# Performance work log

Measured on AMD Instinct MI355X. Metric: run time of the kernel, lower is better.

The kernel has to match this reference:

```python
import jax, jax.numpy as jnp
import numpy as np

K = 15
LAM = 1.0
EPS = 1e-8


def _pdist(a):
    # pairwise euclidean distance (torch.cdist p=2), safe sqrt (zero grad at 0)
    sq = jnp.sum(a * a, axis=1)
    d2 = sq[:, None] + sq[None, :] - 2.0 * (a @ a.T)
    d2 = jnp.maximum(d2, 0.0)
    pos = d2 > 0
    return jnp.where(pos, jnp.sqrt(jnp.where(pos, d2, 1.0)), 0.0)


def _knn_distance_loss(z, xf, k):
    B = xf.shape[0]
    x_dist = _pdist(xf)
    z_dist = _pdist(z)
    eye = jnp.eye(B, dtype=bool)
    x_noself = jnp.where(eye, jnp.inf, x_dist)
    # k smallest per row -> top_k of negated distances
    _, knn_idx = jax.lax.top_k(-x_noself, k)          # (B, k)
    rows = jnp.arange(B)[:, None]
    mask = jnp.zeros((B, B), dtype=bool).at[rows, knn_idx].set(True)
    mask = mask | mask.T                              # symmetric kNN mask
    x_m = jnp.where(mask, x_dist, 0.0)
    z_m = jnp.where(mask, z_dist, 0.0)
    x_norm = x_m / (jnp.max(x_m) + EPS)
    z_norm = z_m / (jnp.max(z_m) + EPS)
    diff2 = jnp.where(mask, (z_norm - x_norm) ** 2, 0.0)
    return diff2.sum() / mask.sum().astype(diff2.dtype)


def _forward(x, We1, be1, We2, be2, Wd1, bd1, Wd2, bd2):
    h = jax.nn.relu(x @ We1 + be1)
    z = h @ We2 + be2                                  # (B, latent)
    h2 = jax.nn.relu(z @ Wd1 + bd1)
    x_rec = h2 @ Wd2 + bd2
    rec_loss = jnp.mean((x_rec - x) ** 2)
    dist_loss = _knn_distance_loss(z, x.reshape(x.shape[0], -1), K)
    return rec_loss + LAM * dist_loss


def setup_inputs() -> dict:
    key = jax.random.key(0)
    ks = jax.random.split(key, 5)
    B, D, H, L = 8192, 1024, 512, 64
    s = 0.02
    return {
        "x": jax.random.normal(ks[0], (B, D), dtype=jnp.float32),
        "We1": jax.random.normal(ks[1], (D, H), dtype=jnp.float32) * s,
        "be1": jnp.zeros((H,), dtype=jnp.float32),
        "We2": jax.random.normal(ks[2], (H, L), dtype=jnp.float32) * s,
        "be2": jnp.zeros((L,), dtype=jnp.float32),
        "Wd1": jax.random.normal(ks[3], (L, H), dtype=jnp.float32) * s,
        "bd1": jnp.zeros((H,), dtype=jnp.float32),
        "Wd2": jax.random.normal(ks[4], (H, D), dtype=jnp.float32) * s,
        "bd2": jnp.zeros((D,), dtype=jnp.float32),
    }


def reference(x, We1, be1, We2, be2, Wd1, bd1, Wd2, bd2):
    return _forward(x, We1, be1, We2, be2, Wd1, bd1, Wd2, bd2)
```

## Files before the change

kernel.cpp:

```cpp
#include <hip/hip_runtime.h>

#define BB 8192
#define DD 1024
#define HH 512
#define LL 64
#define KNN 15
#define NT2 128
#define NTILES2 8256
#define NG1T 1024
#define NBLK2 (NTILES2 + NG1T)
#define CHUNK2 (NBLK2 / 8)
#define SLOTK 8
#define NEDGE (BB * KNN)
#define NEBLK (NEDGE / 128)

typedef __attribute__((ext_vector_type(4))) float f32x4;
typedef __attribute__((ext_vector_type(8))) short s16x8;
typedef __attribute__((ext_vector_type(8))) unsigned short u16x8;
typedef __attribute__((ext_vector_type(4))) unsigned short u16x4;

typedef s16x8 fragT;

__device__ __forceinline__ unsigned short f2bf(float f) {
  unsigned u = __float_as_uint(f);
  return (unsigned short)((u + 0x7fffu + ((u >> 16) & 1u)) >> 16);
}

__device__ __forceinline__ void gload16(const void* g, void* l) {
  __builtin_amdgcn_global_load_lds((const __attribute__((address_space(1))) unsigned int*)g,
                                   (__attribute__((address_space(3))) unsigned int*)l, 16, 0, 0);
}

__device__ __forceinline__ float unpack_d2(unsigned u) {
  _Float16 h = __builtin_bit_cast(_Float16, (unsigned short)(u >> 16));
  return (float)h;
}

__device__ __forceinline__ void ins15(unsigned (&l)[KNN], unsigned u) {
  if (u < l[KNN - 1]) {
    unsigned v = u;
#pragma unroll
    for (int p = 0; p < KNN; ++p) {
      unsigned lo = min(v, l[p]);
      unsigned hi = max(v, l[p]);
      l[p] = lo;
      v = hi;
    }
  }
}

__global__ void k_prep(const float* __restrict__ x, unsigned short* __restrict__ xb,
                       float* __restrict__ sqx,
                       const float* __restrict__ We1, const float* __restrict__ We2,
                       const float* __restrict__ Wd1, const float* __restrict__ Wd2,
                       unsigned short* __restrict__ Wt1, unsigned short* __restrict__ Wt2,
                       unsigned short* __restrict__ Wt3, unsigned short* __restrict__ Wt4) {
  __shared__ float ps[4];
  __shared__ unsigned short T[64][65];
  int b = blockIdx.x;
  int t = threadIdx.x;
  if (b < BB) {
    f32x4 v = *(const f32x4*)(x + (size_t)b * DD + t * 4);
    u16x4 o;
    float s = 0.f;
#pragma unroll
    for (int j = 0; j < 4; ++j) {
      float f = v[j];
      s += f * f;
      o[j] = f2bf(f);
    }
    *(u16x4*)(xb + (size_t)b * DD + t * 4) = o;
#pragma unroll
    for (int off = 32; off >= 1; off >>= 1) s += __shfl_down(s, off);
    if ((t & 63) == 0) ps[t >> 6] = s;
    __syncthreads();
    if (t == 0) sqx[b] = ps[0] + ps[1] + ps[2] + ps[3];
    return;
  }
  int c = b - BB;
  const float* W;
  unsigned short* Wt;
  int Kd, N, idx;
  if (c < 128)      { W = We1; Wt = Wt1; Kd = DD; N = HH; idx = c; }
  else if (c < 136) { W = We2; Wt = Wt2; Kd = HH; N = LL; idx = c - 128; }
  else if (c < 144) { W = Wd1; Wt = Wt3; Kd = LL; N = HH; idx = c - 136; }
  else              { W = Wd2; Wt = Wt4; Kd = HH; N = DD; idx = c - 144; }
  int nx = Kd >> 6;
  int k0 = (idx % nx) * 64, n0 = (idx / nx) * 64;
  int kr = t >> 4, nc = (t & 15) * 4;
#pragma unroll
  for (int q = 0; q < 4; ++q) {
    int k = kr + q * 16;
    f32x4 v = *(const f32x4*)(W + (size_t)(k0 + k) * N + n0 + nc);
#pragma unroll
    for (int j = 0; j < 4; ++j) T[nc + j][k] = f2bf(v[j]);
  }
  __syncthreads();
#pragma unroll
  for (int q = 0; q < 2; ++q) {
    int s = t + q * 256;
    int n = s >> 3, cc = (s & 7) * 8;
    u16x8 o;
#pragma unroll
    for (int j = 0; j < 8; ++j) o[j] = T[n][cc + j];
    *(u16x8*)(Wt + (size_t)(n0 + n) * Kd + k0 + cc) = o;
  }
}

template <int NF, int RELU, int FUSE, int STF32, int STBF>
__device__ __forceinline__ void mgemm_body(
    char* LB, int m0, int n0,
    const unsigned short* __restrict__ A, const unsigned short* __restrict__ Wt,
    const float* __restrict__ bias, unsigned short* __restrict__ Cb, float* __restrict__ Cf,
    const float* __restrict__ Xref, float* __restrict__ rec_sum, int N, int Kd) {
  unsigned short* At = (unsigned short*)LB;
  unsigned short* Bt = (unsigned short*)(LB + 16384);
  int t = threadIdx.x;
  int lane = t & 63, w = t >> 6;
  int wr = w >> 1, wc = w & 1;
  int wbase = w * 64;

  const unsigned short* pA[4];
  const unsigned short* pB[NF];
#pragma unroll
  for (int q = 0; q < 4; ++q) {
    int s = q * 256 + t;
    int r = s >> 3, g = s & 7;
    pA[q] = A + (size_t)(m0 + r) * Kd + (g ^ (r & 7)) * 8;
  }
#pragma unroll
  for (int q = 0; q < NF; ++q) {
    int s = q * 256 + t;
    int r = s >> 3, g = s & 7;
    pB[q] = Wt + (size_t)(n0 + r) * Kd + (g ^ (r & 7)) * 8;
  }

  int lrow = lane & 15;
  int klo = (lane >> 4) << 4;
  int sw = (lane & 7) << 4;

  f32x4 acc[4][NF] = {};

  int ksteps = Kd >> 6;
#pragma unroll
  for (int q = 0; q < 4; ++q) { gload16(pA[q], At + (q * 256 + wbase) * 8); pA[q] += 64; }
#pragma unroll
  for (int q = 0; q < NF; ++q) { gload16(pB[q], Bt + (q * 256 + wbase) * 8); pB[q] += 64; }

  for (int kt = 0; kt < ksteps; ++kt) {
    __syncthreads();
    fragT af[2][4], bf[2][NF];
#pragma unroll
    for (int kh = 0; kh < 2; ++kh) {
      int kbyte = ((kh << 6) | klo) ^ sw;
#pragma unroll
      for (int m = 0; m < 4; ++m)
        af[kh][m] = *(const fragT*)((const char*)At + (wr * 64 + m * 16 + lrow) * 128 + kbyte);
#pragma unroll
      for (int n = 0; n < NF; ++n)
        bf[kh][n] = *(const fragT*)((const char*)Bt + (wc * NF * 16 + n * 16 + lrow) * 128 + kbyte);
    }
    __syncthreads();
    if (kt + 1 < ksteps) {
#pragma unroll
      for (int q = 0; q < 4; ++q) { gload16(pA[q], At + (q * 256 + wbase) * 8); pA[q] += 64; }
#pragma unroll
      for (int q = 0; q < NF; ++q) { gload16(pB[q], Bt + (q * 256 + wbase) * 8); pB[q] += 64; }
    }
#pragma unroll
    for (int kh = 0; kh < 2; ++kh)
#pragma unroll
      for (int m = 0; m < 4; ++m)
#pragma unroll
        for (int n = 0; n < NF; ++n)
          acc[m][n] =
              __builtin_amdgcn_mfma_f32_16x16x32_bf16(af[kh][m], bf[kh][n], acc[m][n], 0, 0, 0);
  }

  float local = 0.f;
#pragma unroll
  for (int m = 0; m < 4; ++m) {
    int row0 = m0 + wr * 64 + m * 16 + ((lane >> 4) << 2);
#pragma unroll
    for (int n = 0; n < NF; ++n) {
      int col = n0 + wc * NF * 16 + n * 16 + lrow;
      float bv = bias[col];
      f32x4 a = acc[m][n];
#pragma unroll
      for (int j = 0; j < 4; ++j) {
        float c = a[j] + bv;
        if (RELU) c = fmaxf(c, 0.f);
        if (FUSE) {
          float xv = Xref[(size_t)(row0 + j) * N + col];
          float d = c - xv;
          local = fmaf(d, d, local);
        }
        if (STBF) Cb[(size_t)(row0 + j) * N + col] = f2bf(c);
        if (STF32) Cf[(size_t)(row0 + j) * N + col] = c;
      }
    }
  }
  if (FUSE) {
#pragma unroll
    for (int off = 32; off >= 1; off >>= 1) local += __shfl_down(local, off);
    __shared__ float rs[4];
    if ((t & 63) == 0) rs[t >> 6] = local;
    __syncthreads();
    if (t == 0) atomicAdd(rec_sum, rs[0] + rs[1] + rs[2] + rs[3]);
  }
}

template <int NF, int RELU, int FUSE, int STF32, int STBF>
__global__ __launch_bounds__(256) void k_mgemm(
    const unsigned short* __restrict__ A, const unsigned short* __restrict__ Wt,
    const float* __restrict__ bias, unsigned short* __restrict__ Cb, float* __restrict__ Cf,
    const float* __restrict__ Xref, float* __restrict__ rec_sum, int N, int Kd) {
  __shared__ __attribute__((aligned(16))) char LB[16384 + NF * 32 * 128];
  mgemm_body<NF, RELU, FUSE, STF32, STBF>(LB, blockIdx.y * 128, blockIdx.x * (NF * 32),
                                          A, Wt, bias, Cb, Cf, Xref, rec_sum, N, Kd);
}

__global__ __launch_bounds__(64, 3) void k_gram64(
    const unsigned short* __restrict__ xb, const float* __restrict__ sqx,
    unsigned* __restrict__ part,
    const unsigned short* __restrict__ Wt1, const float* __restrict__ be1,
    unsigned short* __restrict__ hb) {
  __shared__ __attribute__((aligned(16))) char LB[16384 + 512];
  float* sql = (float*)(LB + 16384);

  int bid = blockIdx.x;
  int b = (bid & 7) * CHUNK2 + (bid >> 3);
  int lane = threadIdx.x;

  int rt, ct;
  bool isG1, diag;
  const unsigned short* Abase;
  const unsigned short* Bbase;
  if (b < NTILES2) {
    isG1 = false;
    float fr = 128.5f - sqrtf(128.5f * 128.5f - 2.0f * (float)b);
    int r = (int)fr;
    while (128 * (r + 1) - ((r + 1) * r) / 2 <= b) ++r;
    while (128 * r - (r * (r - 1)) / 2 > b) --r;
    rt = r;
    ct = r + (b - (128 * r - (r * (r - 1)) / 2));
    diag = (rt == ct);
    Abase = xb + (size_t)rt * 64 * DD;
    Bbase = xb + (size_t)ct * 64 * DD;
  } else {
    isG1 = true;
    diag = false;
    int gg = b - NTILES2;
    rt = gg >> 3;
    ct = gg & 7;
    Abase = xb + (size_t)rt * 64 * DD;
    Bbase = Wt1 + (size_t)ct * 64 * DD;
  }

  if (!isG1) {
    sql[lane] = sqx[rt * 64 + lane];
    sql[64 + lane] = sqx[ct * 64 + lane];
  }
  asm volatile("s_waitcnt vmcnt(0)" ::: "memory");

  const unsigned short* pA[4];
  const unsigned short* pB[4];
#pragma unroll
  for (int q = 0; q < 4; ++q) {
    int s = q * 64 + lane;
    int r = s >> 2;
    int cg = (s & 3) ^ (r & 3);
    pA[q] = Abase + r * DD + cg * 8;
    pB[q] = Bbase + r * DD + cg * 8;
  }

  auto STAGE = [&](int buf) {
    unsigned short* dA = (unsigned short*)(LB + buf * 8192);
    unsigned short* dB = dA + 2048;
#pragma unroll
    for (int q = 0; q < 4; ++q) { gload16(pA[q], dA + q * 512); pA[q] += 32; }
#pragma unroll
    for (int q = 0; q < 4; ++q) { gload16(pB[q], dB + q * 512); pB[q] += 32; }
  };

  STAGE(0);
  STAGE(1);

  int lrow = lane & 15;
  int chx = (lane >> 4) ^ (lane & 3);

  f32x4 acc[4][4] = {};

  for (int kt = 0; kt < 32; ++kt) {
    if (kt < 31) {
      asm volatile("s_waitcnt vmcnt(8)" ::: "memory");
    } else {
      asm volatile("s_waitcnt vmcnt(0)" ::: "memory");
    }
    const char* Ab = (const char*)LB + (kt & 1) * 8192;
    const char* Bb = Ab + 4096;
    fragT af[4], bf[4];
#pragma unroll
    for (int m = 0; m < 4; ++m)
      af[m] = *(const fragT*)(Ab + (m * 16 + lrow) * 64 + chx * 16);
#pragma unroll
    for (int n = 0; n < 4; ++n)
      bf[n] = *(const fragT*)(Bb + (n * 16 + lrow) * 64 + chx * 16);
    asm volatile("s_waitcnt lgkmcnt(0)" ::: "memory");
    __builtin_amdgcn_sched_barrier(0);
    if (kt + 2 < 32) STAGE(kt & 1);
#pragma unroll
    for (int m = 0; m < 4; ++m)
#pragma unroll
      for (int n = 0; n < 4; ++n)
        acc[m][n] = __builtin_amdgcn_mfma_f32_16x16x32_bf16(af[m], bf[n], acc[m][n], 0, 0, 0);
  }

  if (isG1) {
    int n0 = ct * 64;
#pragma unroll
    for (int m = 0; m < 4; ++m)
#pragma unroll
      for (int n = 0; n < 4; ++n) {
        int C = n0 + n * 16 + lrow;
        float bv = be1[C];
        f32x4 a = acc[m][n];
#pragma unroll
        for (int j = 0; j < 4; ++j) {
          int R = rt * 64 + m * 16 + ((lane >> 4) << 2) + j;
          hb[(size_t)R * HH + C] = f2bf(fmaxf(a[j] + bv, 0.f));
        }
      }
    return;
  }

  char* Sf = LB;
#pragma unroll
  for (int m = 0; m < 4; ++m)
#pragma unroll
    for (int n = 0; n < 4; ++n) {
      int C = n * 16 + lrow;
      float sc = sql[64 + C];
      f32x4 a = acc[m][n];
#pragma unroll
      for (int j = 0; j < 4; ++j) {
        int R = m * 16 + ((lane >> 4) << 2) + j;
        float d2 = fmaxf(sql[R] + sc - 2.f * a[j], 0.f);
        if (diag && R == C) d2 = 60000.f;
        *(_Float16*)(Sf + R * 128 + ((C * 2) ^ ((R & 15) << 3))) = (_Float16)d2;
      }
    }
  asm volatile("s_waitcnt lgkmcnt(0)" ::: "memory");
  __builtin_amdgcn_sched_barrier(0);

  unsigned rowlist[KNN];
#pragma unroll
  for (int p = 0; p < KNN; ++p) rowlist[p] = 0xFFFFFFFFu;
  {
    int jb = ct * 64;
    const char* rowp = Sf + lane * 128;
    int swr = (lane & 15) << 3;
    for (int cc = 0; cc < 16; ++cc) {
      u16x4 v4 = *(const u16x4*)(rowp + ((cc * 8) ^ swr));
      unsigned u[4];
#pragma unroll
      for (int q = 0; q < 4; ++q) u[q] = ((unsigned)v4[q] << 16) | (unsigned)(jb + cc * 4 + q);
      unsigned m4 = min(min(u[0], u[1]), min(u[2], u[3]));
      if (m4 < rowlist[KNN - 1]) {
#pragma unroll
        for (int q = 0; q < 4; ++q) ins15(rowlist, u[q]);
      }
    }
  }
  {
    size_t base = (size_t)(ct * SLOTK) * BB + rt * 64 + lane;
#pragma unroll
    for (int p = 0; p < SLOTK; ++p) part[base + (size_t)p * BB] = rowlist[p];
  }

  if (!diag) {
    unsigned collist[KNN];
#pragma unroll
    for (int p = 0; p < KNN; ++p) collist[p] = 0xFFFFFFFFu;
    int ib = rt * 64;
    int c2 = lane * 2;
    for (int rr = 0; rr < 16; ++rr) {
      unsigned u[4];
#pragma unroll
      for (int j = 0; j < 4; ++j) {
        int R = rr * 4 + j;
        unsigned bits = *(const unsigned short*)(Sf + R * 128 + (c2 ^ ((R & 15) << 3)));
        u[j] = (bits << 16) | (unsigned)(ib + R);
      }
      unsigned m4 = min(min(u[0], u[1]), min(u[2], u[3]));
      if (m4 < collist[KNN - 1]) {
#pragma unroll
        for (int j = 0; j < 4; ++j) ins15(collist, u[j]);
      }
    }
    size_t base = (size_t)(rt * SLOTK) * BB + ct * 64 + lane;
#pragma unroll
    for (int p = 0; p < SLOTK; ++p) part[base + (size_t)p * BB] = collist[p];
  }
}

__global__ void k_merge1(const unsigned* __restrict__ part, unsigned* __restrict__ part2) {
  int gid = blockIdx.x * 256 + threadIdx.x;
  int s = gid >> 13, i = gid & 8191;
  unsigned l[KNN];
#pragma unroll
  for (int p = 0; p < KNN; ++p) l[p] = 0xFFFFFFFFu;
  for (int b = s * 16; b < s * 16 + 16; ++b) {
    size_t base = (size_t)(b * SLOTK) * BB + i;
    unsigned u = part[base];
    if (u < l[KNN - 1]) {
      ins15(l, u);
      for (int p = 1; p < SLOTK; ++p) {
        u = part[base + (size_t)p * BB];
        if (u >= l[KNN - 1]) break;
        ins15(l, u);
      }
    }
  }
#pragma unroll
  for (int p = 0; p < KNN; ++p) part2[((size_t)(s * KNN + p)) * BB + i] = l[p];
}

__global__ void k_merge2(const unsigned* __restrict__ part2, float* __restrict__ knn_d2,
                         int* __restrict__ knn_idx, int* __restrict__ xmax_bits) {
  int i = blockIdx.x * 256 + threadIdx.x;
  unsigned l[KNN];
#pragma unroll
  for (int p = 0; p < KNN; ++p) l[p] = 0xFFFFFFFFu;
  for (int q = 0; q < 8; ++q) {
    size_t base = (size_t)(q * KNN) * BB + i;
    unsigned u = part2[base];
    if (u < l[KNN - 1]) {
      ins15(l, u);
      for (int p = 1; p < KNN; ++p) {
        u = part2[base + (size_t)p * BB];
        if (u >= l[KNN - 1]) break;
        ins15(l, u);
      }
    }
  }
  float mx = 0.f;
#pragma unroll
  for (int p = 0; p < KNN; ++p) {
    unsigned u = l[p];
    float d = fmaxf(unpack_d2(u), 0.f);
    mx = fmaxf(mx, d);
    knn_d2[(size_t)i * KNN + p] = d;
    knn_idx[(size_t)i * KNN + p] = (int)(u & 0xFFFFu);
  }
  int t = threadIdx.x;
#pragma unroll
  for (int off = 32; off >= 1; off >>= 1) mx = fmaxf(mx, __shfl_down(mx, off));
  __shared__ float rm[4];
  if ((t & 63) == 0) rm[t >> 6] = mx;
  __syncthreads();
  if (t == 0) {
    float mb = fmaxf(fmaxf(rm[0], rm[1]), fmaxf(rm[2], rm[3]));
    atomicMax(xmax_bits, __float_as_int(mb));
  }
}

__global__ void k_edge(const float* __restrict__ z, const int* __restrict__ knn_idx,
                       const float* __restrict__ knn_d2, float* __restrict__ pzz,
                       float* __restrict__ pxx, float* __restrict__ pxz,
                       float* __restrict__ pcnt, float* __restrict__ pzm) {
  int t = threadIdx.x;
  int g = t >> 4, L = t & 15;
  int lane = t & 63;
  float szz = 0.f, sxx = 0.f, sxz = 0.f, scnt = 0.f, zm = 0.f;
#pragma unroll
  for (int pass = 0; pass < 8; ++pass) {
    int e = blockIdx.x * 128 + pass * 16 + g;
    int i = e / KNN;
    int j = knn_idx[e];
    f32x4 zi = *(const f32x4*)(z + (size_t)i * LL + L * 4);
    f32x4 zj = *(const f32x4*)(z + (size_t)j * LL + L * 4);
    float v = 0.f;
#pragma unroll
    for (int d = 0; d < 4; ++d) {
      float df = zi[d] - zj[d];
      v = fmaf(df, df, v);
    }
    v += __shfl_down(v, 8);
    v += __shfl_down(v, 4);
    v += __shfl_down(v, 2);
    v += __shfl_down(v, 1);
    int cand = (L < KNN) ? knn_idx[(size_t)j * KNN + L] : -1;
    unsigned long long ball = __ballot(cand == i);
    unsigned recip = (unsigned)(ball >> (lane & 48)) & 0xFFFFu;
    if (L == 0) {
      float w = recip ? 1.f : 2.f;
      float xd2 = knn_d2[e];
      szz = fmaf(w, v, szz);
      sxx = fmaf(w, xd2, sxx);
      sxz = fmaf(w, sqrtf(v * xd2), sxz);
      scnt += w;
      zm = fmaxf(zm, v);
    }
  }
#pragma unroll
  for (int off = 32; off >= 1; off >>= 1) {
    szz += __shfl_down(szz, off);
    sxx += __shfl_down(sxx, off);
    sxz += __shfl_down(sxz, off);
    scnt += __shfl_down(scnt, off);
    zm = fmaxf(zm, __shfl_down(zm, off));
  }
  __shared__ float r[5][4];
  int w4 = t >> 6;
  if (lane == 0) {
    r[0][w4] = szz; r[1][w4] = sxx; r[2][w4] = sxz; r[3][w4] = scnt; r[4][w4] = zm;
  }
  __syncthreads();
  if (t == 0) {
    pzz[blockIdx.x] = r[0][0] + r[0][1] + r[0][2] + r[0][3];
    pxx[blockIdx.x] = r[1][0] + r[1][1] + r[1][2] + r[1][3];
    pxz[blockIdx.x] = r[2][0] + r[2][1] + r[2][2] + r[2][3];
    pcnt[blockIdx.x] = r[3][0] + r[3][1] + r[3][2] + r[3][3];
    pzm[blockIdx.x] = fmaxf(fmaxf(r[4][0], r[4][1]), fmaxf(r[4][2], r[4][3]));
  }
}

__global__ void k_final(const float* __restrict__ pzz, const float* __restrict__ pxx,
                        const float* __restrict__ pxz, const float* __restrict__ pcnt,
                        const float* __restrict__ pzm, const int* __restrict__ xmax_bits,
                        const float* __restrict__ rec_sum, float* __restrict__ out) {
  int t = threadIdx.x;
  float szz = 0.f, sxx = 0.f, sxz = 0.f, scnt = 0.f, zm = 0.f;
  for (int bb = t; bb < NEBLK; bb += 256) {
    szz += pzz[bb];
    sxx += pxx[bb];
    sxz += pxz[bb];
    scnt += pcnt[bb];
    zm = fmaxf(zm, pzm[bb]);
  }
#pragma unroll
  for (int off = 32; off >= 1; off >>= 1) {
    szz += __shfl_down(szz, off);
    sxx += __shfl_down(sxx, off);
    sxz += __shfl_down(sxz, off);
    scnt += __shfl_down(scnt, off);
    zm = fmaxf(zm, __shfl_down(zm, off));
  }
  __shared__ float r[5][4];
  int w4 = t >> 6;
  if ((t & 63) == 0) {
    r[0][w4] = szz; r[1][w4] = sxx; r[2][w4] = sxz; r[3][w4] = scnt; r[4][w4] = zm;
  }
  __syncthreads();
  if (t == 0) {
    float SZZ = r[0][0] + r[0][1] + r[0][2] + r[0][3];
    float SXX = r[1][0] + r[1][1] + r[1][2] + r[1][3];
    float SXZ = r[2][0] + r[2][1] + r[2][2] + r[2][3];
    float CNT = r[3][0] + r[3][1] + r[3][2] + r[3][3];
    float ZM = fmaxf(fmaxf(r[4][0], r[4][1]), fmaxf(r[4][2], r[4][3]));
    float xmax = __int_as_float(*xmax_bits);
    float a = 1.f / (sqrtf(ZM) + 1e-8f);
    float bq = 1.f / (sqrtf(xmax) + 1e-8f);
    float loss = (a * a * SZZ + bq * bq * SXX - 2.f * a * bq * SXZ) / CNT;
    out[0] = rec_sum[0] * (1.f / 8388608.f) + loss;
  }
}

extern "C" void kernel_launch(void* const* d_in, const int* in_sizes, int n_in,
                              void* d_out, int out_size, void* d_ws, size_t ws_size,
                              hipStream_t stream) {
  const float* x = (const float*)d_in[0];
  const float* We1 = (const float*)d_in[1];
  const float* be1 = (const float*)d_in[2];
  const float* We2 = (const float*)d_in[3];
  const float* be2 = (const float*)d_in[4];
  const float* Wd1 = (const float*)d_in[5];
  const float* bd1 = (const float*)d_in[6];
  const float* Wd2 = (const float*)d_in[7];
  const float* bd2 = (const float*)d_in[8];

  char* ws = (char*)d_ws;
  size_t off = 0;
  auto alloc = [&](size_t bytes) {
    void* p = ws + off;
    off += (bytes + 255) & ~(size_t)255;
    return p;
  };
  unsigned short* xb = (unsigned short*)alloc((size_t)BB * DD * 2);
  unsigned short* hb = (unsigned short*)alloc((size_t)BB * HH * 2);
  unsigned short* zb = (unsigned short*)alloc((size_t)BB * LL * 2);
  unsigned short* h2b = (unsigned short*)alloc((size_t)BB * HH * 2);
  float* z = (float*)alloc((size_t)BB * LL * 4);
  float* sqx = (float*)alloc((size_t)BB * 4);
  unsigned short* Wt1 = (unsigned short*)alloc((size_t)HH * DD * 2);
  unsigned short* Wt2 = (unsigned short*)alloc((size_t)LL * HH * 2);
  unsigned short* Wt3 = (unsigned short*)alloc((size_t)HH * LL * 2);
  unsigned short* Wt4 = (unsigned short*)alloc((size_t)DD * HH * 2);
  unsigned* part = (unsigned*)alloc((size_t)NT2 * SLOTK * BB * 4);
  unsigned* part2 = (unsigned*)alloc((size_t)8 * KNN * BB * 4);
  float* knn_d2 = (float*)alloc((size_t)BB * KNN * 4);
  int* knn_idx = (int*)alloc((size_t)BB * KNN * 4);
  float* pzz = (float*)alloc(NEBLK * 4);
  float* pxx = (float*)alloc(NEBLK * 4);
  float* pxz = (float*)alloc(NEBLK * 4);
  float* pcnt = (float*)alloc(NEBLK * 4);
  float* pzm = (float*)alloc(NEBLK * 4);
  float* scal = (float*)alloc(64);
  float* rec_sum = scal + 0;
  int* xmax_bits = (int*)(scal + 1);

  hipMemsetAsync(scal, 0, 64, stream);

  k_prep<<<BB + 272, 256, 0, stream>>>(x, xb, sqx, We1, We2, Wd1, Wd2, Wt1, Wt2, Wt3, Wt4);

  k_gram64<<<NBLK2, 64, 0, stream>>>(xb, sqx, part, Wt1, be1, hb);

  k_mgemm<2, 0, 0, 1, 1><<<dim3(LL / 64, BB / 128), 256, 0, stream>>>(
      hb, Wt2, be2, zb, z, nullptr, nullptr, LL, HH);
  k_mgemm<4, 1, 0, 0, 1><<<dim3(HH / 128, BB / 128), 256, 0, stream>>>(
      zb, Wt3, bd1, h2b, nullptr, nullptr, nullptr, HH, LL);
  k_mgemm<4, 0, 1, 0, 0><<<dim3(DD / 128, BB / 128), 256, 0, stream>>>(
      h2b, Wt4, bd2, nullptr, nullptr, x, rec_sum, DD, HH);

  k_merge1<<<256, 256, 0, stream>>>(part, part2);
  k_merge2<<<BB / 256, 256, 0, stream>>>(part2, knn_d2, knn_idx, xmax_bits);
  k_edge<<<NEBLK, 256, 0, stream>>>(z, knn_idx, knn_d2, pzz, pxx, pxz, pcnt, pzm);
  k_final<<<1, 256, 0, stream>>>(pzz, pxx, pxz, pcnt, pzm, xmax_bits, rec_sum, (float*)d_out);
}
```

Before: 327.3 us.

## Load gram fragments directly to registers and co-schedule tail kernels

```diff
diff --git a/kernel.cpp b/kernel.cpp
--- a/kernel.cpp
+++ b/kernel.cpp
@@ -210,23 +210,13 @@
   }
 }
 
-template <int NF, int RELU, int FUSE, int STF32, int STBF>
-__global__ __launch_bounds__(256) void k_mgemm(
-    const unsigned short* __restrict__ A, const unsigned short* __restrict__ Wt,
-    const float* __restrict__ bias, unsigned short* __restrict__ Cb, float* __restrict__ Cf,
-    const float* __restrict__ Xref, float* __restrict__ rec_sum, int N, int Kd) {
-  __shared__ __attribute__((aligned(16))) char LB[16384 + NF * 32 * 128];
-  mgemm_body<NF, RELU, FUSE, STF32, STBF>(LB, blockIdx.y * 128, blockIdx.x * (NF * 32),
-                                          A, Wt, bias, Cb, Cf, Xref, rec_sum, N, Kd);
-}
-
 __global__ __launch_bounds__(64, 3) void k_gram64(
     const unsigned short* __restrict__ xb, const float* __restrict__ sqx,
     unsigned* __restrict__ part,
     const unsigned short* __restrict__ Wt1, const float* __restrict__ be1,
     unsigned short* __restrict__ hb) {
-  __shared__ __attribute__((aligned(16))) char LB[16384 + 512];
-  float* sql = (float*)(LB + 16384);
+  __shared__ __attribute__((aligned(16))) char LB[8192 + 512];
+  float* sql = (float*)(LB + 8192);
 
   int bid = blockIdx.x;
   int b = (bid & 7) * CHUNK2 + (bid >> 3);
@@ -261,59 +251,52 @@
     sql[lane] = sqx[rt * 64 + lane];
     sql[64 + lane] = sqx[ct * 64 + lane];
   }
-  asm volatile("s_waitcnt vmcnt(0)" ::: "memory");
-
-  const unsigned short* pA[4];
-  const unsigned short* pB[4];
-#pragma unroll
-  for (int q = 0; q < 4; ++q) {
-    int s = q * 64 + lane;
-    int r = s >> 2;
-    int cg = (s & 3) ^ (r & 3);
-    pA[q] = Abase + r * DD + cg * 8;
-    pB[q] = Bbase + r * DD + cg * 8;
-  }
-
-  auto STAGE = [&](int buf) {
-    unsigned short* dA = (unsigned short*)(LB + buf * 8192);
-    unsigned short* dB = dA + 2048;
-#pragma unroll
-    for (int q = 0; q < 4; ++q) { gload16(pA[q], dA + q * 512); pA[q] += 32; }
-#pragma unroll
-    for (int q = 0; q < 4; ++q) { gload16(pB[q], dB + q * 512); pB[q] += 32; }
-  };
-
-  STAGE(0);
-  STAGE(1);
 
   int lrow = lane & 15;
-  int chx = (lane >> 4) ^ (lane & 3);
-
+  int ch = lane >> 4;
+
+  const unsigned short* ap[4];
+  const unsigned short* bp[4];
+#pragma unroll
+  for (int m = 0; m < 4; ++m) {
+    ap[m] = Abase + (m * 16 + lrow) * DD + ch * 8;
+    bp[m] = Bbase + (m * 16 + lrow) * DD + ch * 8;
+  }
+
+  fragT a0[4], b0[4], a1[4], b1[4];
   f32x4 acc[4][4] = {};
 
-  for (int kt = 0; kt < 32; ++kt) {
-    if (kt < 31) {
-      asm volatile("s_waitcnt vmcnt(8)" ::: "memory");
-    } else {
-      asm volatile("s_waitcnt vmcnt(0)" ::: "memory");
-    }
-    const char* Ab = (const char*)LB + (kt & 1) * 8192;
-    const char* Bb = Ab + 4096;
-    fragT af[4], bf[4];
-#pragma unroll
-    for (int m = 0; m < 4; ++m)
-      af[m] = *(const fragT*)(Ab + (m * 16 + lrow) * 64 + chx * 16);
+#pragma unroll
+  for (int m = 0; m < 4; ++m) {
+    a0[m] = *(const fragT*)(ap[m]);
+    b0[m] = *(const fragT*)(bp[m]);
+  }
+
+  for (int kt = 0; kt < 32; kt += 2) {
+    int ko = (kt + 1) * 32;
+#pragma unroll
+    for (int m = 0; m < 4; ++m) {
+      a1[m] = *(const fragT*)(ap[m] + ko);
+      b1[m] = *(const fragT*)(bp[m] + ko);
+    }
 #pragma unroll
     for (int n = 0; n < 4; ++n)
-      bf[n] = *(const fragT*)(Bb + (n * 16 + lrow) * 64 + chx * 16);
-    asm volatile("s_waitcnt lgkmcnt(0)" ::: "memory");
-    __builtin_amdgcn_sched_barrier(0);
-    if (kt + 2 < 32) STAGE(kt & 1);
-#pragma unroll
-    for (int m = 0; m < 4; ++m)
-#pragma unroll
-      for (int n = 0; n < 4; ++n)
-        acc[m][n] = __builtin_amdgcn_mfma_f32_16x16x32_bf16(af[m], bf[n], acc[m][n], 0, 0, 0);
+#pragma unroll
+      for (int m = 0; m < 4; ++m)
+        acc[m][n] = __builtin_amdgcn_mfma_f32_16x16x32_bf16(a0[m], b0[n], acc[m][n], 0, 0, 0);
+    if (kt + 2 < 32) {
+      int ko2 = (kt + 2) * 32;
+#pragma unroll
+      for (int m = 0; m < 4; ++m) {
+        a0[m] = *(const fragT*)(ap[m] + ko2);
+        b0[m] = *(const fragT*)(bp[m] + ko2);
+      }
+    }
+#pragma unroll
+    for (int n = 0; n < 4; ++n)
+#pragma unroll
+      for (int m = 0; m < 4; ++m)
+        acc[m][n] = __builtin_amdgcn_mfma_f32_16x16x32_bf16(a1[m], b1[n], acc[m][n], 0, 0, 0);
   }
 
   if (isG1) {
@@ -404,8 +387,8 @@
   }
 }
 
-__global__ void k_merge1(const unsigned* __restrict__ part, unsigned* __restrict__ part2) {
-  int gid = blockIdx.x * 256 + threadIdx.x;
+__device__ __forceinline__ void merge1_body(int gid, const unsigned* __restrict__ part,
+                                            unsigned* __restrict__ part2) {
   int s = gid >> 13, i = gid & 8191;
   unsigned l[KNN];
 #pragma unroll
@@ -426,9 +409,9 @@
   for (int p = 0; p < KNN; ++p) part2[((size_t)(s * KNN + p)) * BB + i] = l[p];
 }
 
-__global__ void k_merge2(const unsigned* __restrict__ part2, float* __restrict__ knn_d2,
-                         int* __restrict__ knn_idx, int* __restrict__ xmax_bits) {
-  int i = blockIdx.x * 256 + threadIdx.x;
+__device__ __forceinline__ void merge2_body(int i, const unsigned* __restrict__ part2,
+                                            float* __restrict__ knn_d2, int* __restrict__ knn_idx,
+                                            int* __restrict__ xmax_bits) {
   unsigned l[KNN];
 #pragma unroll
   for (int p = 0; p < KNN; ++p) l[p] = 0xFFFFFFFFu;
@@ -465,17 +448,19 @@
   }
 }
 
-__global__ void k_edge(const float* __restrict__ z, const int* __restrict__ knn_idx,
-                       const float* __restrict__ knn_d2, float* __restrict__ pzz,
-                       float* __restrict__ pxx, float* __restrict__ pxz,
-                       float* __restrict__ pcnt, float* __restrict__ pzm) {
+__device__ __forceinline__ void edge_body(int eb, const float* __restrict__ z,
+                                          const int* __restrict__ knn_idx,
+                                          const float* __restrict__ knn_d2,
+                                          float* __restrict__ pzz, float* __restrict__ pxx,
+                                          float* __restrict__ pxz, float* __restrict__ pcnt,
+                                          float* __restrict__ pzm) {
   int t = threadIdx.x;
   int g = t >> 4, L = t & 15;
   int lane = t & 63;
   float szz = 0.f, sxx = 0.f, sxz = 0.f, scnt = 0.f, zm = 0.f;
 #pragma unroll
   for (int pass = 0; pass < 8; ++pass) {
-    int e = blockIdx.x * 128 + pass * 16 + g;
+    int e = eb * 128 + pass * 16 + g;
     int i = e / KNN;
     int j = knn_idx[e];
     f32x4 zi = *(const f32x4*)(z + (size_t)i * LL + L * 4);
@@ -518,11 +503,55 @@
   }
   __syncthreads();
   if (t == 0) {
-    pzz[blockIdx.x] = r[0][0] + r[0][1] + r[0][2] + r[0][3];
-    pxx[blockIdx.x] = r[1][0] + r[1][1] + r[1][2] + r[1][3];
-    pxz[blockIdx.x] = r[2][0] + r[2][1] + r[2][2] + r[2][3];
-    pcnt[blockIdx.x] = r[3][0] + r[3][1] + r[3][2] + r[3][3];
-    pzm[blockIdx.x] = fmaxf(fmaxf(r[4][0], r[4][1]), fmaxf(r[4][2], r[4][3]));
+    pzz[eb] = r[0][0] + r[0][1] + r[0][2] + r[0][3];
+    pxx[eb] = r[1][0] + r[1][1] + r[1][2] + r[1][3];
+    pxz[eb] = r[2][0] + r[2][1] + r[2][2] + r[2][3];
+    pcnt[eb] = r[3][0] + r[3][1] + r[3][2] + r[3][3];
+    pzm[eb] = fmaxf(fmaxf(r[4][0], r[4][1]), fmaxf(r[4][2], r[4][3]));
+  }
+}
+
+__global__ __launch_bounds__(256) void k_tail2(
+    const unsigned short* __restrict__ hb, const unsigned short* __restrict__ Wt2,
+    const float* __restrict__ be2, unsigned short* __restrict__ zb, float* __restrict__ z,
+    const unsigned* __restrict__ part, unsigned* __restrict__ part2) {
+  __shared__ __attribute__((aligned(16))) char LB[16384 + 8192];
+  int bid = blockIdx.x;
+  if (bid < 64) {
+    mgemm_body<2, 0, 0, 1, 1>(LB, bid * 128, 0, hb, Wt2, be2, zb, z, nullptr, nullptr, LL, HH);
+  } else {
+    merge1_body((bid - 64) * 256 + threadIdx.x, part, part2);
+  }
+}
+
+__global__ __launch_bounds__(256) void k_tail3(
+    const unsigned short* __restrict__ zb, const unsigned short* __restrict__ Wt3,
+    const float* __restrict__ bd1, unsigned short* __restrict__ h2b,
+    const unsigned* __restrict__ part2, float* __restrict__ knn_d2, int* __restrict__ knn_idx,
+    int* __restrict__ xmax_bits) {
+  __shared__ __attribute__((aligned(16))) char LB[16384 + 16384];
+  int bid = blockIdx.x;
+  if (bid < 256) {
+    mgemm_body<4, 1, 0, 0, 1>(LB, (bid >> 2) * 128, (bid & 3) * 128, zb, Wt3, bd1, h2b, nullptr,
+                              nullptr, nullptr, HH, LL);
+  } else {
+    merge2_body((bid - 256) * 256 + threadIdx.x, part2, knn_d2, knn_idx, xmax_bits);
+  }
+}
+
+__global__ __launch_bounds__(256) void k_tail4(
+    const unsigned short* __restrict__ h2b, const unsigned short* __restrict__ Wt4,
+    const float* __restrict__ bd2, const float* __restrict__ x, float* __restrict__ rec_sum,
+    const float* __restrict__ z, const int* __restrict__ knn_idx,
+    const float* __restrict__ knn_d2, float* __restrict__ pzz, float* __restrict__ pxx,
+    float* __restrict__ pxz, float* __restrict__ pcnt, float* __restrict__ pzm) {
+  __shared__ __attribute__((aligned(16))) char LB[16384 + 16384];
+  int bid = blockIdx.x;
+  if (bid < 512) {
+    mgemm_body<4, 0, 1, 0, 0>(LB, (bid >> 3) * 128, (bid & 7) * 128, h2b, Wt4, bd2, nullptr,
+                              nullptr, x, rec_sum, DD, HH);
+  } else {
+    edge_body(bid - 512, z, knn_idx, knn_d2, pzz, pxx, pxz, pcnt, pzm);
   }
 }
 
@@ -616,15 +645,9 @@
 
   k_gram64<<<NBLK2, 64, 0, stream>>>(xb, sqx, part, Wt1, be1, hb);
 
-  k_mgemm<2, 0, 0, 1, 1><<<dim3(LL / 64, BB / 128), 256, 0, stream>>>(
-      hb, Wt2, be2, zb, z, nullptr, nullptr, LL, HH);
-  k_mgemm<4, 1, 0, 0, 1><<<dim3(HH / 128, BB / 128), 256, 0, stream>>>(
-      zb, Wt3, bd1, h2b, nullptr, nullptr, nullptr, HH, LL);
-  k_mgemm<4, 0, 1, 0, 0><<<dim3(DD / 128, BB / 128), 256, 0, stream>>>(
-      h2b, Wt4, bd2, nullptr, nullptr, x, rec_sum, DD, HH);
-
-  k_merge1<<<256, 256, 0, stream>>>(part, part2);
-  k_merge2<<<BB / 256, 256, 0, stream>>>(part2, knn_d2, knn_idx, xmax_bits);
-  k_edge<<<NEBLK, 256, 0, stream>>>(z, knn_idx, knn_d2, pzz, pxx, pxz, pcnt, pzm);
+  k_tail2<<<64 + 256, 256, 0, stream>>>(hb, Wt2, be2, zb, z, part, part2);
+  k_tail3<<<256 + 32, 256, 0, stream>>>(zb, Wt3, bd1, h2b, part2, knn_d2, knn_idx, xmax_bits);
+  k_tail4<<<512 + NEBLK, 256, 0, stream>>>(h2b, Wt4, bd2, x, rec_sum, z, knn_idx, knn_d2,
+                                           pzz, pxx, pxz, pcnt, pzm);
   k_final<<<1, 256, 0, stream>>>(pzz, pxx, pxz, pcnt, pzm, xmax_bits, rec_sum, (float*)d_out);
 }
```

New measurement: 458.1 us. +40.0%, slower.
